# Kernel optimization log

Measured on AMD Instinct MI355X. Metric: run time of the kernel, lower is better.

Reference implementation:

```python
import jax, jax.numpy as jnp
import numpy as np

B, L, D = 4, 512, 768
NUM_SPANS = 4096
MAX_WIDTH = 8
DFF = 4 * D


def setup_inputs() -> dict:
    key = jax.random.key(0)
    k_h, k_s, k_w, k1, k2 = jax.random.split(key, 5)
    h = jax.random.normal(k_h, (B, L, D), dtype=jnp.float32)
    starts = jax.random.randint(k_s, (B, NUM_SPANS), 0, L)
    widths = jax.random.randint(k_w, (B, NUM_SPANS), 1, MAX_WIDTH + 1)
    ends = jnp.minimum(starts + widths - 1, L - 1)
    span_idx = jnp.stack([starts, ends], axis=-1).astype(jnp.int64 if jax.config.jax_enable_x64 else jnp.int32)
    W1 = jax.random.normal(k1, (D, DFF), dtype=jnp.float32) * (1.0 / np.sqrt(D))
    b1 = jnp.zeros((DFF,), dtype=jnp.float32)
    W2 = jax.random.normal(k2, (DFF, D), dtype=jnp.float32) * (1.0 / np.sqrt(DFF))
    b2 = jnp.zeros((D,), dtype=jnp.float32)
    return {"h": h, "span_idx": span_idx, "W1": W1, "b1": b1, "W2": W2, "b2": b2,
            "max_width": MAX_WIDTH}


def reference(h, span_idx, W1, b1, W2, b2, max_width):
    # h: [B, L, D]; span_idx: [B, S, 2] (start, end inclusive)
    Bv, Lv, Dv = h.shape
    starts = span_idx[:, :, 0]                       # [B, S]
    lengths = span_idx[:, :, 1] - starts + 1         # [B, S]
    offsets = jnp.arange(max_width)                  # static bound on span length
    positions = starts[:, :, None] + offsets[None, None, :]      # [B, S, W]
    mask = offsets[None, None, :] < lengths[:, :, None]          # [B, S, W]
    positions = jnp.clip(positions * mask, 0, Lv - 1)
    # indexed gather-reduce (no [B,S,L,D] broadcast): [B, S, W, D]
    gathered = h[jnp.arange(Bv)[:, None, None], positions]
    summed = jnp.sum(gathered * mask[..., None].astype(h.dtype), axis=2)  # [B, S, D]
    span_reps = summed / lengths[..., None].astype(h.dtype)
    # projection: Linear -> ReLU -> (Dropout: identity at eval) -> Linear
    hmid = jax.nn.relu(jnp.einsum('bsd,df->bsf', span_reps, W1) + b1)
    out = jnp.einsum('bsf,fd->bsd', hmid, W2) + b2
    return out
```

## Files before the change

### kernel.cpp

```cpp
#include <hip/hip_runtime.h>
#include <stdint.h>

#define B_DIM 4
#define L_DIM 512
#define D_DIM 768
#define S_DIM 4096
#define DFF_DIM 3072
#define M_DIM (B_DIM * S_DIM)

typedef unsigned short ushort_t;
typedef __attribute__((ext_vector_type(8))) short short8;
typedef __attribute__((ext_vector_type(4))) short short4v;
typedef __attribute__((ext_vector_type(4))) float floatx4;

__device__ __forceinline__ ushort_t f2bf(float x) {
  unsigned int u = __float_as_uint(x);
  u += 0x7FFFu + ((u >> 16) & 1u);
  return (ushort_t)(u >> 16);
}

__device__ __forceinline__ void load_lds16(const ushort_t* g, ushort_t* lds) {
  __builtin_amdgcn_global_load_lds(
      (const __attribute__((address_space(1))) unsigned int*)g,
      (__attribute__((address_space(3))) unsigned int*)lds, 16, 0, 0);
}

#define PIN() __builtin_amdgcn_sched_barrier(0)
#define BAR()                                  \
  do {                                         \
    PIN();                                     \
    __builtin_amdgcn_s_barrier();              \
    PIN();                                     \
  } while (0)
#define WAIT_LGKM0()                           \
  do {                                         \
    asm volatile("s_waitcnt lgkmcnt(0)");      \
    PIN();                                     \
  } while (0)
#define WAIT_VM(n)                             \
  do {                                         \
    asm volatile("s_waitcnt vmcnt(" #n ")");   \
    PIN();                                     \
  } while (0)

__device__ __forceinline__ void transpose_body(const float* __restrict__ in,
                                               ushort_t* __restrict__ out,
                                               int K, int N, int kb, int nb) {
  __shared__ float tile[32][33];
  const int k0 = kb * 32;
  const int n0 = nb * 32;
  const int tx = threadIdx.x & 31;
  const int ty = threadIdx.x >> 5;
#pragma unroll
  for (int r = 0; r < 32; r += 8)
    tile[ty + r][tx] = in[(long)(k0 + ty + r) * N + n0 + tx];
  __syncthreads();
#pragma unroll
  for (int r = 0; r < 32; r += 8)
    out[(long)(n0 + ty + r) * K + k0 + tx] = f2bf(tile[tx][ty + r]);
}

__device__ __forceinline__ void span_body(const float* __restrict__ h,
                                          const int* __restrict__ span_idx,
                                          ushort_t* __restrict__ A, int blk) {
  const int wave = threadIdx.x >> 6;
  const int lane = threadIdx.x & 63;
  const int span = blk * 4 + wave;
  const int b = span >> 12;
  const int start = span_idx[span * 2 + 0];
  const int end   = span_idx[span * 2 + 1];
  const float inv = 1.0f / (float)(end - start + 1);
  const floatx4* hb =
      (const floatx4*)(h + ((long)b * L_DIM + start) * D_DIM) + lane;
  floatx4 a[3];
#pragma unroll
  for (int c = 0; c < 3; ++c) a[c] = (floatx4)0.0f;
  for (int p = start; p <= end; ++p) {
#pragma unroll
    for (int c = 0; c < 3; ++c) a[c] += hb[c * 64];
    hb += 192;
  }
  short4v* o = (short4v*)(A + (long)span * D_DIM) + lane;
#pragma unroll
  for (int c = 0; c < 3; ++c) {
    short4v s;
#pragma unroll
    for (int e = 0; e < 4; ++e) s[e] = (short)f2bf(a[c][e] * inv);
    o[c * 64] = s;
  }
}

__global__ __launch_bounds__(256)
void prep(const float* __restrict__ W1, ushort_t* __restrict__ W1T,
          const float* __restrict__ W2, ushort_t* __restrict__ W2T,
          const float* __restrict__ h, const int* __restrict__ span_idx,
          ushort_t* __restrict__ A) {
  const int blk = blockIdx.x;
  if (blk < 2304) {
    transpose_body(W1, W1T, D_DIM, DFF_DIM, blk % 24, blk / 24);
  } else if (blk < 4608) {
    const int b = blk - 2304;
    transpose_body(W2, W2T, DFF_DIM, D_DIM, b % 96, b / 96);
  } else {
    span_body(h, span_idx, A, blk - 4608);
  }
}

__global__ __launch_bounds__(512, 2)
void gemm1_p3(const ushort_t* __restrict__ A, const ushort_t* __restrict__ Bt,
              const float* __restrict__ bias, ushort_t* __restrict__ C) {
  __shared__ ushort_t As[3][128 * 64];
  __shared__ ushort_t Bs[3][256 * 64];

  const int tid  = threadIdx.x;
  const int lane = tid & 63;
  const int l16  = lane & 15;
  const int quad = lane >> 4;
  const int wave = tid >> 6;
  const int wr   = wave >> 2;
  const int wc   = wave & 3;

  const int bm = blockIdx.x;
  const int bn = blockIdx.y;

  const int srow = tid >> 3;
  const int gch  = (tid & 7) ^ (srow & 7);
  const ushort_t* gA = A  + (long)(bm * 128 + srow) * 768 + gch * 8;
  const ushort_t* gB = Bt + (long)(bn * 256 + srow) * 768 + gch * 8;
  const long r64 = (long)768 * 64;

  auto STAGE_A = [&](int buf, int kt) {
    const long ko = (long)kt * 64;
    ushort_t* la = &As[buf][0] + tid * 8;
    load_lds16(gA + ko,       la);
    load_lds16(gA + ko + r64, la + 4096);
  };
  auto STAGE_B01 = [&](int buf, int kt) {
    const long ko = (long)kt * 64;
    ushort_t* lb = &Bs[buf][0] + tid * 8;
    load_lds16(gB + ko,       lb);
    load_lds16(gB + ko + r64, lb + 4096);
  };
  auto STAGE_B23 = [&](int buf, int kt) {
    const long ko = (long)kt * 64;
    ushort_t* lb = &Bs[buf][0] + tid * 8;
    load_lds16(gB + ko + 2 * r64, lb + 8192);
    load_lds16(gB + ko + 3 * r64, lb + 12288);
  };

  const int arow0 = (wr * 64 + l16) * 64;
  const int brow0 = (wc * 64 + l16) * 64;
  const int cx0 = ((quad)     ^ (l16 & 7)) << 3;
  const int cx1 = ((quad + 4) ^ (l16 & 7)) << 3;

  floatx4 acc[4][4];
#pragma unroll
  for (int i = 0; i < 4; ++i)
#pragma unroll
    for (int j = 0; j < 4; ++j) acc[i][j] = (floatx4)0.0f;

  const int nk = 12;

  STAGE_A(0, 0); STAGE_B01(0, 0); STAGE_B23(0, 0);
  STAGE_A(1, 1); STAGE_B01(1, 1); STAGE_B23(1, 1);
  WAIT_VM(6);
  BAR();

  short8 a0[2][2], a2[2][2], b0[2][2], b2[2][2];
  int cur = 0;

  for (int k = 0; k < nk; ++k) {
    const int s2 = (cur + 2 >= 3) ? cur - 1 : cur + 2;
    const ushort_t* Ac = &As[cur][0];
    const ushort_t* Bc = &Bs[cur][0];
    const bool pf = (k + 2 < nk);

#pragma unroll
    for (int i = 0; i < 2; ++i) {
      a0[i][0] = *(const short8*)(Ac + arow0 + i * 1024 + cx0);
      a0[i][1] = *(const short8*)(Ac + arow0 + i * 1024 + cx1);
    }
#pragma unroll
    for (int j = 0; j < 2; ++j) {
      b0[j][0] = *(const short8*)(Bc + brow0 + j * 1024 + cx0);
      b0[j][1] = *(const short8*)(Bc + brow0 + j * 1024 + cx1);
    }
    if (pf) STAGE_A(s2, k + 2);
    BAR();
    WAIT_LGKM0();
    __builtin_amdgcn_s_setprio(1);
#pragma unroll
    for (int i = 0; i < 2; ++i)
#pragma unroll
      for (int j = 0; j < 2; ++j) {
        acc[i][j] = __builtin_amdgcn_mfma_f32_16x16x32_bf16(a0[i][0], b0[j][0], acc[i][j], 0, 0, 0);
        acc[i][j] = __builtin_amdgcn_mfma_f32_16x16x32_bf16(a0[i][1], b0[j][1], acc[i][j], 0, 0, 0);
      }
    __builtin_amdgcn_s_setprio(0);

#pragma unroll
    for (int j = 0; j < 2; ++j) {
      b2[j][0] = *(const short8*)(Bc + brow0 + (2 + j) * 1024 + cx0);
      b2[j][1] = *(const short8*)(Bc + brow0 + (2 + j) * 1024 + cx1);
    }
    if (pf) STAGE_B01(s2, k + 2);
    BAR();
    WAIT_LGKM0();
    __builtin_amdgcn_s_setprio(1);
#pragma unroll
    for (int i = 0; i < 2; ++i)
#pragma unroll
      for (int j = 0; j < 2; ++j) {
        acc[i][2 + j] = __builtin_amdgcn_mfma_f32_16x16x32_bf16(a0[i][0], b2[j][0], acc[i][2 + j], 0, 0, 0);
        acc[i][2 + j] = __builtin_amdgcn_mfma_f32_16x16x32_bf16(a0[i][1], b2[j][1], acc[i][2 + j], 0, 0, 0);
      }
    __builtin_amdgcn_s_setprio(0);

#pragma unroll
    for (int i = 0; i < 2; ++i) {
      a2[i][0] = *(const short8*)(Ac + arow0 + (2 + i) * 1024 + cx0);
      a2[i][1] = *(const short8*)(Ac + arow0 + (2 + i) * 1024 + cx1);
    }
    if (pf) STAGE_B23(s2, k + 2);
    BAR();
    WAIT_LGKM0();
    __builtin_amdgcn_s_setprio(1);
#pragma unroll
    for (int i = 0; i < 2; ++i)
#pragma unroll
      for (int j = 0; j < 2; ++j) {
        acc[2 + i][2 + j] = __builtin_amdgcn_mfma_f32_16x16x32_bf16(a2[i][0], b2[j][0], acc[2 + i][2 + j], 0, 0, 0);
        acc[2 + i][2 + j] = __builtin_amdgcn_mfma_f32_16x16x32_bf16(a2[i][1], b2[j][1], acc[2 + i][2 + j], 0, 0, 0);
      }
    __builtin_amdgcn_s_setprio(0);

    if (pf) {
      WAIT_VM(6);
    } else {
      WAIT_VM(0);
    }
    BAR();
    __builtin_amdgcn_s_setprio(1);
#pragma unroll
    for (int i = 0; i < 2; ++i)
#pragma unroll
      for (int j = 0; j < 2; ++j) {
        acc[2 + i][j] = __builtin_amdgcn_mfma_f32_16x16x32_bf16(a2[i][0], b0[j][0], acc[2 + i][j], 0, 0, 0);
        acc[2 + i][j] = __builtin_amdgcn_mfma_f32_16x16x32_bf16(a2[i][1], b0[j][1], acc[2 + i][j], 0, 0, 0);
      }
    __builtin_amdgcn_s_setprio(0);

    cur = (cur + 1 >= 3) ? 0 : cur + 1;
  }

  const long rowbase = (long)bm * 128 + wr * 64 + quad * 4;
  const int  colbase = bn * 256 + wc * 64 + l16;
#pragma unroll
  for (int j = 0; j < 4; ++j) {
    const int col = colbase + j * 16;
    const float bv = bias[col];
#pragma unroll
    for (int i = 0; i < 4; ++i) {
      const long row0 = rowbase + i * 16;
#pragma unroll
      for (int r = 0; r < 4; ++r) {
        float v = acc[i][j][r] + bv;
        v = v > 0.0f ? v : 0.0f;
        C[(row0 + r) * DFF_DIM + col] = f2bf(v);
      }
    }
  }
}

template <int MODE>
__global__ __launch_bounds__(256)
void gemm_bt(const ushort_t* __restrict__ A, const ushort_t* __restrict__ Bt,
             const float* __restrict__ bias, void* __restrict__ Cv,
             int M, int N, int K) {
  __shared__ ushort_t As[2][128 * 32];
  __shared__ ushort_t Bs[2][128 * 32];

  const int tid  = threadIdx.x;
  const int lane = tid & 63;
  const int wave = tid >> 6;
  const int l16  = lane & 15;
  const int quad = lane >> 4;

  const int bm = blockIdx.x;
  const int bn = blockIdx.y;

  const int wm = (wave & 1) * 64;
  const int wn = (wave >> 1) * 64;

  const int swz  = (l16 & 3) ^ ((l16 >> 2) & 3);
  const int coff = (quad ^ swz) * 8;

  floatx4 acc[4][4];
#pragma unroll
  for (int i = 0; i < 4; ++i)
#pragma unroll
    for (int j = 0; j < 4; ++j)
      acc[i][j] = (floatx4)0.0f;

  const int s0 = tid, s1 = tid + 256;
  const int r0 = s0 >> 2, r1 = s1 >> 2;
  const int c0 = (s0 & 3) ^ (r0 & 3) ^ ((r0 >> 2) & 3);
  const int c1 = (s1 & 3) ^ (r1 & 3) ^ ((r1 >> 2) & 3);
  const ushort_t* gA0 = A + (long)(bm * 128 + r0) * K + c0 * 8;
  const ushort_t* gA1 = A + (long)(bm * 128 + r1) * K + c1 * 8;
  const ushort_t* gB0 = Bt + (long)(bn * 128 + r0) * K + c0 * 8;
  const ushort_t* gB1 = Bt + (long)(bn * 128 + r1) * K + c1 * 8;

  const int nk = K >> 5;

  load_lds16(gA0, &As[0][0] + s0 * 8);
  load_lds16(gA1, &As[0][0] + s1 * 8);
  load_lds16(gB0, &Bs[0][0] + s0 * 8);
  load_lds16(gB1, &Bs[0][0] + s1 * 8);

  for (int k = 0; k < nk; ++k) {
    const int cur = k & 1;
    const int nxt = cur ^ 1;
    __syncthreads();

    if (k + 1 < nk) {
      const int off = (k + 1) * 32;
      load_lds16(gA0 + off, &As[nxt][0] + s0 * 8);
      load_lds16(gA1 + off, &As[nxt][0] + s1 * 8);
      load_lds16(gB0 + off, &Bs[nxt][0] + s0 * 8);
      load_lds16(gB1 + off, &Bs[nxt][0] + s1 * 8);
    }

    short8 af[4], bf[4];
#pragma unroll
    for (int i = 0; i < 4; ++i)
      af[i] = *(const short8*)(&As[cur][0] + (wm + i * 16 + l16) * 32 + coff);
#pragma unroll
    for (int j = 0; j < 4; ++j)
      bf[j] = *(const short8*)(&Bs[cur][0] + (wn + j * 16 + l16) * 32 + coff);
#pragma unroll
    for (int i = 0; i < 4; ++i)
#pragma unroll
      for (int j = 0; j < 4; ++j)
        acc[i][j] = __builtin_amdgcn_mfma_f32_16x16x32_bf16(af[i], bf[j], acc[i][j], 0, 0, 0);
  }

#pragma unroll
  for (int i = 0; i < 4; ++i) {
#pragma unroll
    for (int j = 0; j < 4; ++j) {
      const int col = bn * 128 + wn + j * 16 + l16;
      const float bv = bias[col];
      const int row0 = bm * 128 + wm + i * 16 + quad * 4;
#pragma unroll
      for (int r = 0; r < 4; ++r) {
        float v = acc[i][j][r] + bv;
        if (MODE == 0) {
          v = v > 0.0f ? v : 0.0f;
          ((ushort_t*)Cv)[(long)(row0 + r) * N + col] = f2bf(v);
        } else {
          ((float*)Cv)[(long)(row0 + r) * N + col] = v;
        }
      }
    }
  }
}

extern "C" void kernel_launch(void* const* d_in, const int* in_sizes, int n_in,
                              void* d_out, int out_size, void* d_ws, size_t ws_size,
                              hipStream_t stream) {
  const float* h        = (const float*)d_in[0];
  const int*   span_idx = (const int*)d_in[1];
  const float* W1       = (const float*)d_in[2];
  const float* b1       = (const float*)d_in[3];
  const float* W2       = (const float*)d_in[4];
  const float* b2       = (const float*)d_in[5];
  float* out = (float*)d_out;

  ushort_t* A   = (ushort_t*)d_ws;
  ushort_t* W1T = A + (size_t)M_DIM * D_DIM;
  ushort_t* W2T = W1T + (size_t)DFF_DIM * D_DIM;
  ushort_t* Hm  = W2T + (size_t)D_DIM * DFF_DIM;

  prep<<<2304 + 2304 + M_DIM / 4, 256, 0, stream>>>(W1, W1T, W2, W2T, h, span_idx, A);

  gemm1_p3<<<dim3(M_DIM / 128, DFF_DIM / 256), 512, 0, stream>>>(A, W1T, b1, Hm);

  gemm_bt<1><<<dim3(M_DIM / 128, D_DIM / 128), 256, 0, stream>>>(
      Hm, W2T, b2, out, M_DIM, D_DIM, DFF_DIM);
}
```

Measured before the change: 275.1 us.

## Use prefix-sum span pooling and a 256x256-tile first GEMM

Adds a column-wise prefix-sum kernel over h so each span mean becomes a difference of two prefix rows instead of a loop over up to eight rows. The first GEMM is replaced with a 256x256 tile kernel using a K-step of 32, a triple-buffered LDS pipeline and an 8x4 accumulator grid per wave, which raises data reuse per block. The scan runs on only 12 blocks with a serial loop over 512 positions, which may add latency. The prefix buffer reuses the Hm workspace region, and prefix differences in fp32 can lose some precision.

```diff
diff --git a/kernel.cpp b/kernel.cpp
--- a/kernel.cpp
+++ b/kernel.cpp
@@ -43,6 +43,26 @@
     PIN();                                     \
   } while (0)
 
+__global__ __launch_bounds__(256)
+void scan(const float* __restrict__ h, float* __restrict__ P) {
+  const int g = blockIdx.x * 256 + threadIdx.x;
+  const int b = g / D_DIM;
+  const int d = g - b * D_DIM;
+  const float* src = h + (long)b * L_DIM * D_DIM + d;
+  float* dst = P + (long)b * L_DIM * D_DIM + d;
+  float run = 0.0f;
+  for (int l = 0; l < L_DIM; l += 8) {
+    float v[8];
+#pragma unroll
+    for (int u = 0; u < 8; ++u) v[u] = src[(long)(l + u) * D_DIM];
+#pragma unroll
+    for (int u = 0; u < 8; ++u) {
+      run += v[u];
+      dst[(long)(l + u) * D_DIM] = run;
+    }
+  }
+}
+
 __device__ __forceinline__ void transpose_body(const float* __restrict__ in,
                                                ushort_t* __restrict__ out,
                                                int K, int N, int kb, int nb) {
@@ -60,7 +80,7 @@
     out[(long)(n0 + ty + r) * K + k0 + tx] = f2bf(tile[tx][ty + r]);
 }
 
-__device__ __forceinline__ void span_body(const float* __restrict__ h,
+__device__ __forceinline__ void span_body(const float* __restrict__ P,
                                           const int* __restrict__ span_idx,
                                           ushort_t* __restrict__ A, int blk) {
   const int wave = threadIdx.x >> 6;
@@ -70,30 +90,30 @@
   const int start = span_idx[span * 2 + 0];
   const int end   = span_idx[span * 2 + 1];
   const float inv = 1.0f / (float)(end - start + 1);
-  const floatx4* hb =
-      (const floatx4*)(h + ((long)b * L_DIM + start) * D_DIM) + lane;
-  floatx4 a[3];
-#pragma unroll
-  for (int c = 0; c < 3; ++c) a[c] = (floatx4)0.0f;
-  for (int p = start; p <= end; ++p) {
-#pragma unroll
-    for (int c = 0; c < 3; ++c) a[c] += hb[c * 64];
-    hb += 192;
+  const floatx4* Pb = (const floatx4*)(P + (long)b * L_DIM * D_DIM);
+  const floatx4* Pe = Pb + (long)end * 192 + lane;
+  floatx4 s[3];
+#pragma unroll
+  for (int c = 0; c < 3; ++c) s[c] = Pe[c * 64];
+  if (start > 0) {
+    const floatx4* Ps = Pb + (long)(start - 1) * 192 + lane;
+#pragma unroll
+    for (int c = 0; c < 3; ++c) s[c] -= Ps[c * 64];
   }
   short4v* o = (short4v*)(A + (long)span * D_DIM) + lane;
 #pragma unroll
   for (int c = 0; c < 3; ++c) {
-    short4v s;
-#pragma unroll
-    for (int e = 0; e < 4; ++e) s[e] = (short)f2bf(a[c][e] * inv);
-    o[c * 64] = s;
+    short4v v;
+#pragma unroll
+    for (int e = 0; e < 4; ++e) v[e] = (short)f2bf(s[c][e] * inv);
+    o[c * 64] = v;
   }
 }
 
 __global__ __launch_bounds__(256)
 void prep(const float* __restrict__ W1, ushort_t* __restrict__ W1T,
           const float* __restrict__ W2, ushort_t* __restrict__ W2T,
-          const float* __restrict__ h, const int* __restrict__ span_idx,
+          const float* __restrict__ P, const int* __restrict__ span_idx,
           ushort_t* __restrict__ A) {
   const int blk = blockIdx.x;
   if (blk < 2304) {
@@ -102,15 +122,15 @@
     const int b = blk - 2304;
     transpose_body(W2, W2T, DFF_DIM, D_DIM, b % 96, b / 96);
   } else {
-    span_body(h, span_idx, A, blk - 4608);
+    span_body(P, span_idx, A, blk - 4608);
   }
 }
 
 __global__ __launch_bounds__(512, 2)
-void gemm1_p3(const ushort_t* __restrict__ A, const ushort_t* __restrict__ Bt,
-              const float* __restrict__ bias, ushort_t* __restrict__ C) {
-  __shared__ ushort_t As[3][128 * 64];
-  __shared__ ushort_t Bs[3][256 * 64];
+void gemm_sb(const ushort_t* __restrict__ A, const ushort_t* __restrict__ Bt,
+             const float* __restrict__ bias, ushort_t* __restrict__ C) {
+  __shared__ ushort_t As[3][256 * 32];
+  __shared__ ushort_t Bs[3][256 * 32];
 
   const int tid  = threadIdx.x;
   const int lane = tid & 63;
@@ -123,50 +143,45 @@
   const int bm = blockIdx.x;
   const int bn = blockIdx.y;
 
-  const int srow = tid >> 3;
-  const int gch  = (tid & 7) ^ (srow & 7);
-  const ushort_t* gA = A  + (long)(bm * 128 + srow) * 768 + gch * 8;
-  const ushort_t* gB = Bt + (long)(bn * 256 + srow) * 768 + gch * 8;
-  const long r64 = (long)768 * 64;
+  const int K = D_DIM;
+  const int nk = 24;
+
+  const int s0 = tid, s1 = tid + 512;
+  const int r0 = s0 >> 2, r1 = s1 >> 2;
+  const int c0 = (s0 & 3) ^ (r0 & 3) ^ ((r0 >> 2) & 3);
+  const int c1 = (s1 & 3) ^ (r1 & 3) ^ ((r1 >> 2) & 3);
+  const ushort_t* gA0 = A + (long)(bm * 256 + r0) * K + c0 * 8;
+  const ushort_t* gA1 = A + (long)(bm * 256 + r1) * K + c1 * 8;
+  const ushort_t* gB0 = Bt + (long)(bn * 256 + r0) * K + c0 * 8;
+  const ushort_t* gB1 = Bt + (long)(bn * 256 + r1) * K + c1 * 8;
 
   auto STAGE_A = [&](int buf, int kt) {
-    const long ko = (long)kt * 64;
-    ushort_t* la = &As[buf][0] + tid * 8;
-    load_lds16(gA + ko,       la);
-    load_lds16(gA + ko + r64, la + 4096);
+    const int ko = kt * 32;
+    load_lds16(gA0 + ko, &As[buf][0] + s0 * 8);
+    load_lds16(gA1 + ko, &As[buf][0] + s1 * 8);
   };
-  auto STAGE_B01 = [&](int buf, int kt) {
-    const long ko = (long)kt * 64;
-    ushort_t* lb = &Bs[buf][0] + tid * 8;
-    load_lds16(gB + ko,       lb);
-    load_lds16(gB + ko + r64, lb + 4096);
+  auto STAGE_B = [&](int buf, int kt) {
+    const int ko = kt * 32;
+    load_lds16(gB0 + ko, &Bs[buf][0] + s0 * 8);
+    load_lds16(gB1 + ko, &Bs[buf][0] + s1 * 8);
   };
-  auto STAGE_B23 = [&](int buf, int kt) {
-    const long ko = (long)kt * 64;
-    ushort_t* lb = &Bs[buf][0] + tid * 8;
-    load_lds16(gB + ko + 2 * r64, lb + 8192);
-    load_lds16(gB + ko + 3 * r64, lb + 12288);
-  };
-
-  const int arow0 = (wr * 64 + l16) * 64;
-  const int brow0 = (wc * 64 + l16) * 64;
-  const int cx0 = ((quad)     ^ (l16 & 7)) << 3;
-  const int cx1 = ((quad + 4) ^ (l16 & 7)) << 3;
-
-  floatx4 acc[4][4];
-#pragma unroll
-  for (int i = 0; i < 4; ++i)
+
+  const int coff = ((quad ^ (l16 & 3) ^ ((l16 >> 2) & 3))) * 8;
+  const int arow0 = (wr * 128 + l16) * 32;
+  const int brow0 = (wc * 64 + l16) * 32;
+
+  floatx4 acc[8][4];
+#pragma unroll
+  for (int i = 0; i < 8; ++i)
 #pragma unroll
     for (int j = 0; j < 4; ++j) acc[i][j] = (floatx4)0.0f;
 
-  const int nk = 12;
-
-  STAGE_A(0, 0); STAGE_B01(0, 0); STAGE_B23(0, 0);
-  STAGE_A(1, 1); STAGE_B01(1, 1); STAGE_B23(1, 1);
-  WAIT_VM(6);
+  STAGE_A(0, 0); STAGE_B(0, 0);
+  STAGE_A(1, 1); STAGE_B(1, 1);
+  WAIT_VM(4);
   BAR();
 
-  short8 a0[2][2], a2[2][2], b0[2][2], b2[2][2];
+  short8 af[4], af2[4], bf[4];
   int cur = 0;
 
   for (int k = 0; k < nk; ++k) {
@@ -176,91 +191,52 @@
     const bool pf = (k + 2 < nk);
 
 #pragma unroll
-    for (int i = 0; i < 2; ++i) {
-      a0[i][0] = *(const short8*)(Ac + arow0 + i * 1024 + cx0);
-      a0[i][1] = *(const short8*)(Ac + arow0 + i * 1024 + cx1);
-    }
-#pragma unroll
-    for (int j = 0; j < 2; ++j) {
-      b0[j][0] = *(const short8*)(Bc + brow0 + j * 1024 + cx0);
-      b0[j][1] = *(const short8*)(Bc + brow0 + j * 1024 + cx1);
-    }
-    if (pf) STAGE_A(s2, k + 2);
+    for (int i = 0; i < 4; ++i)
+      af[i] = *(const short8*)(Ac + arow0 + i * 512 + coff);
+#pragma unroll
+    for (int j = 0; j < 4; ++j)
+      bf[j] = *(const short8*)(Bc + brow0 + j * 512 + coff);
     BAR();
     WAIT_LGKM0();
     __builtin_amdgcn_s_setprio(1);
 #pragma unroll
-    for (int i = 0; i < 2; ++i)
-#pragma unroll
-      for (int j = 0; j < 2; ++j) {
-        acc[i][j] = __builtin_amdgcn_mfma_f32_16x16x32_bf16(a0[i][0], b0[j][0], acc[i][j], 0, 0, 0);
-        acc[i][j] = __builtin_amdgcn_mfma_f32_16x16x32_bf16(a0[i][1], b0[j][1], acc[i][j], 0, 0, 0);
-      }
+    for (int i = 0; i < 4; ++i)
+#pragma unroll
+      for (int j = 0; j < 4; ++j)
+        acc[i][j] = __builtin_amdgcn_mfma_f32_16x16x32_bf16(af[i], bf[j], acc[i][j], 0, 0, 0);
     __builtin_amdgcn_s_setprio(0);
 
 #pragma unroll
-    for (int j = 0; j < 2; ++j) {
-      b2[j][0] = *(const short8*)(Bc + brow0 + (2 + j) * 1024 + cx0);
-      b2[j][1] = *(const short8*)(Bc + brow0 + (2 + j) * 1024 + cx1);
-    }
-    if (pf) STAGE_B01(s2, k + 2);
+    for (int i = 0; i < 4; ++i)
+      af2[i] = *(const short8*)(Ac + arow0 + (4 + i) * 512 + coff);
+    if (pf) {
+      STAGE_A(s2, k + 2);
+      STAGE_B(s2, k + 2);
+      WAIT_VM(4);
+    } else {
+      WAIT_VM(0);
+    }
     BAR();
     WAIT_LGKM0();
     __builtin_amdgcn_s_setprio(1);
 #pragma unroll
-    for (int i = 0; i < 2; ++i)
-#pragma unroll
-      for (int j = 0; j < 2; ++j) {
-        acc[i][2 + j] = __builtin_amdgcn_mfma_f32_16x16x32_bf16(a0[i][0], b2[j][0], acc[i][2 + j], 0, 0, 0);
-        acc[i][2 + j] = __builtin_amdgcn_mfma_f32_16x16x32_bf16(a0[i][1], b2[j][1], acc[i][2 + j], 0, 0, 0);
-      }
+    for (int i = 0; i < 4; ++i)
+#pragma unroll
+      for (int j = 0; j < 4; ++j)
+        acc[4 + i][j] = __builtin_amdgcn_mfma_f32_16x16x32_bf16(af2[i], bf[j], acc[4 + i][j], 0, 0, 0);
     __builtin_amdgcn_s_setprio(0);
 
-#pragma unroll
-    for (int i = 0; i < 2; ++i) {
-      a2[i][0] = *(const short8*)(Ac + arow0 + (2 + i) * 1024 + cx0);
-      a2[i][1] = *(const short8*)(Ac + arow0 + (2 + i) * 1024 + cx1);
-    }
-    if (pf) STAGE_B23(s2, k + 2);
-    BAR();
-    WAIT_LGKM0();
-    __builtin_amdgcn_s_setprio(1);
-#pragma unroll
-    for (int i = 0; i < 2; ++i)
-#pragma unroll
-      for (int j = 0; j < 2; ++j) {
-        acc[2 + i][2 + j] = __builtin_amdgcn_mfma_f32_16x16x32_bf16(a2[i][0], b2[j][0], acc[2 + i][2 + j], 0, 0, 0);
-        acc[2 + i][2 + j] = __builtin_amdgcn_mfma_f32_16x16x32_bf16(a2[i][1], b2[j][1], acc[2 + i][2 + j], 0, 0, 0);
-      }
-    __builtin_amdgcn_s_setprio(0);
-
-    if (pf) {
-      WAIT_VM(6);
-    } else {
-      WAIT_VM(0);
-    }
-    BAR();
-    __builtin_amdgcn_s_setprio(1);
-#pragma unroll
-    for (int i = 0; i < 2; ++i)
-#pragma unroll
-      for (int j = 0; j < 2; ++j) {
-        acc[2 + i][j] = __builtin_amdgcn_mfma_f32_16x16x32_bf16(a2[i][0], b0[j][0], acc[2 + i][j], 0, 0, 0);
-        acc[2 + i][j] = __builtin_amdgcn_mfma_f32_16x16x32_bf16(a2[i][1], b0[j][1], acc[2 + i][j], 0, 0, 0);
-      }
-    __builtin_amdgcn_s_setprio(0);
-
     cur = (cur + 1 >= 3) ? 0 : cur + 1;
   }
 
-  const long rowbase = (long)bm * 128 + wr * 64 + quad * 4;
+  const long rowbase = (long)bm * 256 + wr * 128 + quad * 4;
   const int  colbase = bn * 256 + wc * 64 + l16;
 #pragma unroll
   for (int j = 0; j < 4; ++j) {
     const int col = colbase + j * 16;
     const float bv = bias[col];
 #pragma unroll
-    for (int i = 0; i < 4; ++i) {
+    for (int i = 0; i < 8; ++i) {
       const long row0 = rowbase + i * 16;
 #pragma unroll
       for (int r = 0; r < 4; ++r) {
@@ -382,9 +358,13 @@
   ushort_t* W2T = W1T + (size_t)DFF_DIM * D_DIM;
   ushort_t* Hm  = W2T + (size_t)D_DIM * DFF_DIM;
 
-  prep<<<2304 + 2304 + M_DIM / 4, 256, 0, stream>>>(W1, W1T, W2, W2T, h, span_idx, A);
-
-  gemm1_p3<<<dim3(M_DIM / 128, DFF_DIM / 256), 512, 0, stream>>>(A, W1T, b1, Hm);
+  float* P = (float*)Hm;
+
+  scan<<<12, 256, 0, stream>>>(h, P);
+
+  prep<<<2304 + 2304 + M_DIM / 4, 256, 0, stream>>>(W1, W1T, W2, W2T, P, span_idx, A);
+
+  gemm_sb<<<dim3(64, 12), 512, 0, stream>>>(A, W1T, b1, Hm);
 
   gemm_bt<1><<<dim3(M_DIM / 128, D_DIM / 128), 256, 0, stream>>>(
       Hm, W2T, b2, out, M_DIM, D_DIM, DFF_DIM);
```

New measurement: 301.6 us. 1.1x slower.
